# Kernel optimization log

Measured on AMD Instinct MI355X. Metric: run time of the kernel, lower is better.

The kernel has to match this reference:

```python
import jax, jax.numpy as jnp
import numpy as np

B, N, K, C, CM = 4, 1024, 9, 32, 128
SIGMA = 1.0
EPS = 1e-5
SLOPE = 0.01  # LeakyReLU default negative slope


def _batchnorm(x, gamma, beta):
    # training-mode BatchNorm1d over the point dimension
    m = x.mean(axis=0)
    v = x.var(axis=0)
    return gamma * (x - m) * jax.lax.rsqrt(v + EPS) + beta


def setup_inputs() -> dict:
    key = jax.random.key(0)
    ks = jax.random.split(key, 8)
    positions = jax.random.uniform(ks[0], (B * N, 2), jnp.float32) * 10.0
    weights = jax.random.normal(ks[1], (B * N, C), jnp.float32)
    # learned kernel offsets (grid-init in original; random offsets of same scale here)
    kernel_pos = jax.random.normal(ks[2], (K, 2), jnp.float32) * (2.0 * SIGMA)
    conv_w = jax.random.normal(ks[3], (K, C, C), jnp.float32) / np.sqrt(K * C)
    w1 = jax.random.normal(ks[4], (C, CM), jnp.float32) / np.sqrt(C)
    w2 = jax.random.normal(ks[5], (CM, C), jnp.float32) / np.sqrt(CM)
    return {
        "positions": positions,
        "weights": weights,
        "kernel_pos": kernel_pos,
        "conv_w": conv_w,
        "bn_gamma": jnp.ones((C,), jnp.float32),
        "bn_beta": jnp.zeros((C,), jnp.float32),
        "w1": w1,
        "b1": jnp.zeros((CM,), jnp.float32),
        "bn1_gamma": jnp.ones((CM,), jnp.float32),
        "bn1_beta": jnp.zeros((CM,), jnp.float32),
        "w2": w2,
        "b2": jnp.zeros((C,), jnp.float32),
        "n_batch": B,
        "n_points": N,
    }


def reference(positions, weights, kernel_pos, conv_w, bn_gamma, bn_beta,
              w1, b1, bn1_gamma, bn1_beta, w2, b2, n_batch, n_points):
    b, n = n_batch, n_points
    k = kernel_pos.shape[0]
    c = weights.shape[-1]
    pos = positions.reshape(b, n, 2)
    w = weights.reshape(b, n, c)

    # KernelConv: each component spawns K shifted components with channel mixing
    comp_pos = pos[:, :, None, :] + kernel_pos[None, None, :, :]      # [b,n,k,2]
    comp_w = jnp.einsum('bnc,kcd->bnkd', w, conv_w)                   # [b,n,k,c]

    # KernelSample: evaluate the resulting Gaussian mixture at the input positions
    diff = pos[:, :, None, None, :] - comp_pos[:, None, :, :, :]      # [b,i,n,k,2]
    dist2 = jnp.sum(diff * diff, axis=-1)                             # [b,i,n,k]
    kmat = jnp.exp(-dist2 / (2.0 * SIGMA * SIGMA))
    y = jnp.einsum('bink,bnkc->bic', kmat, comp_w)                    # [b,i,c]
    y = jax.nn.leaky_relu(y, SLOPE)
    y = y.reshape(b * n, c)

    # conv_norm + residual add of input weights
    y = _batchnorm(y, bn_gamma, bn_beta)
    y = y + weights

    # PyG MLP [C, CM, C], act_first=True, plain_last=True
    h = y @ w1 + b1
    h = jax.nn.leaky_relu(h, SLOPE)
    h = _batchnorm(h, bn1_gamma, bn1_beta)
    delta = h @ w2 + b2

    return y + delta  # output weights [b*n, c]; positions pass through unchanged
```

## Files before the change

kernel.cpp:

```cpp
#include <hip/hip_runtime.h>

#define BB 4
#define NN 1024
#define KK 9
#define C  32
#define CM 128
#define M  (BB*NN)
#define EPSB 1e-5f
#define SLOPE 0.01f

#define KPAD 296
#define WTS  40
#define GST  296
#define CWS  288

typedef _Float16 f16x8 __attribute__((ext_vector_type(8)));
typedef _Float16 f16x4 __attribute__((ext_vector_type(4)));
typedef float    f32x4 __attribute__((ext_vector_type(4)));

__device__ __forceinline__ float leaky(float x){ return x > 0.f ? x : SLOPE*x; }

__device__ __forceinline__ float fexp2(float x){
#if __has_builtin(__builtin_amdgcn_exp2f)
  return __builtin_amdgcn_exp2f(x);
#else
  return exp2f(x);
#endif
}

__global__ __launch_bounds__(512) void k2_main(const float* __restrict__ pos,
                                               const float* __restrict__ wts,
                                               const float* __restrict__ kpos,
                                               const float* __restrict__ conv_w,
                                               float* __restrict__ z,
                                               float* __restrict__ zpart,
                                               float* __restrict__ stats){
  __shared__ __align__(16) char smem[57984];
  _Float16* wT0 = (_Float16*)smem;
  float*    pnl = (float*)(smem + 5120);
  _Float16* km0 = (_Float16*)(smem + 13312);
  float* gld  = (float*)smem;
  float* cwT  = (float*)(smem + 18944);
  float* red2 = (float*)(smem + 55808);

  int bid = blockIdx.x;
  int b = bid >> 6, it = bid & 63;
  int tid = threadIdx.x;
  int lane = tid & 63, wid = tid >> 6;
  int mm = lane & 15, quad = lane >> 4;
  int c0 = (wid & 1) * 16, q = wid >> 1;
  int gk = tid >> 7, ig = (tid >> 3) & 15, np = tid & 7;
  int wn = tid >> 4, wc = (tid & 15) * 2;

  if (bid == 0){ for (int i = tid; i < 256; i += 512) stats[i] = 0.f; }

  const float BETA = -0.72134752f;
  float Ak[KK], Bk[KK], Ck[KK];
  #pragma unroll
  for (int k = 0; k < KK; ++k){
    float kxx = kpos[2*k], kyy = kpos[2*k+1];
    Ak[k] = -2.f*BETA*kxx;
    Bk[k] = -2.f*BETA*kyy;
    Ck[k] = BETA*(kxx*kxx + kyy*kyy);
  }

  const float2* wch = (const float2*)(wts + (size_t)b*NN*C);

#define WWRITE(dst, L) do{ \
    (dst)[wc*WTS + wn]     = (_Float16)(L).x; \
    (dst)[(wc+1)*WTS + wn] = (_Float16)(L).y; \
  }while(0)

#define GEN(dst, ss) do{ \
    float dx_[4], dy_[4], e0_[4]; \
    _Pragma("unroll") \
    for (int jj = 0; jj < 4; ++jj){ \
      int nl_ = np*4 + jj; \
      dx_[jj] = pix - pnl[2*((ss)*32 + nl_)]; \
      dy_[jj] = piy - pnl[2*((ss)*32 + nl_) + 1]; \
      e0_[jj] = BETA*(dx_[jj]*dx_[jj] + dy_[jj]*dy_[jj]); \
    } \
    _Pragma("unroll") \
    for (int t_ = 0; t_ < 3; ++t_){ \
      int k_ = gk + t_*4; \
      if (k_ < KK){ \
        f16x4 ev_; \
        _Pragma("unroll") \
        for (int jj = 0; jj < 4; ++jj){ \
          float x_ = (e0_[jj] + Ck[k_]) + dx_[jj]*Ak[k_] + dy_[jj]*Bk[k_]; \
          ev_[jj] = (_Float16)fexp2(x_); \
        } \
        *(f16x4*)&(dst)[ig*KPAD + k_*32 + np*4] = ev_; \
      } \
    } \
  }while(0)

  ((float4*)pnl)[tid] = ((const float4*)(pos + (size_t)b*NN*2))[tid];
  float2 L0 = wch[tid];
  float2 Ln = wch[512 + tid];
  WWRITE(wT0, L0);
  __syncthreads();
  float pix = pnl[2*(it*16 + ig)];
  float piy = pnl[2*(it*16 + ig) + 1];
  GEN(km0, 0);
  asm volatile("s_waitcnt lgkmcnt(0)" ::: "memory");
  __builtin_amdgcn_s_barrier();
  __builtin_amdgcn_sched_barrier(0);

  f32x4 acc0 = {0.f,0.f,0.f,0.f}, acc1 = {0.f,0.f,0.f,0.f}, acc2 = {0.f,0.f,0.f,0.f};
  for (int s = 0; s < 32; ++s){
    int cur = s & 1;
    if (s < 31){
      float2 Lw = Ln;
      if (s < 30) Ln = wch[(size_t)(s+2)*512 + tid];
      _Float16* wTn = wT0 + (cur^1)*(32*WTS);
      WWRITE(wTn, Lw);
      _Float16* kmn = km0 + (cur^1)*(16*KPAD);
      GEN(kmn, s+1);
    }
    const _Float16* kmc = km0 + cur*(16*KPAD);
    const _Float16* wTc = wT0 + cur*(32*WTS);
    f16x8 bf = *(const f16x8*)&wTc[(c0+mm)*WTS + quad*8];
    f16x8 a0 = *(const f16x8*)&kmc[mm*KPAD + (q+0)*32 + quad*8];
    acc0 = __builtin_amdgcn_mfma_f32_16x16x32_f16(a0, bf, acc0, 0, 0, 0);
    f16x8 a1 = *(const f16x8*)&kmc[mm*KPAD + (q+4)*32 + quad*8];
    acc1 = __builtin_amdgcn_mfma_f32_16x16x32_f16(a1, bf, acc1, 0, 0, 0);
    if (q == 0){
      f16x8 a2 = *(const f16x8*)&kmc[mm*KPAD + 8*32 + quad*8];
      acc2 = __builtin_amdgcn_mfma_f32_16x16x32_f16(a2, bf, acc2, 0, 0, 0);
    }
    asm volatile("s_waitcnt lgkmcnt(0)" ::: "memory");
    __builtin_amdgcn_sched_barrier(0);
    __builtin_amdgcn_s_barrier();
    __builtin_amdgcn_sched_barrier(0);
  }
#undef WWRITE
#undef GEN

  #pragma unroll
  for (int r = 0; r < 4; ++r){
    gld[(quad*4+r)*GST + (q+0)*32 + c0+mm] = acc0[r];
    gld[(quad*4+r)*GST + (q+4)*32 + c0+mm] = acc1[r];
  }
  if (q == 0){
    #pragma unroll
    for (int r = 0; r < 4; ++r)
      gld[(quad*4+r)*GST + 8*32 + c0+mm] = acc2[r];
  }
  for (int v = tid; v < (KK*C*C)/4; v += 512){
    float4 cv = ((const float4*)conv_w)[v];
    int f = v*4;
    int kc = f >> 5;
    int cb = f & 31;
    int q4 = kc >> 2, sub = kc & 3;
    #pragma unroll
    for (int j = 0; j < 4; ++j){
      int c = cb + j;
      cwT[c*CWS + ((q4 ^ (c & 7))<<2) + sub] = (&cv.x)[j];
    }
  }
  __syncthreads();

  int rr = tid >> 5, cc = tid & 31;
  const float4* g4 = (const float4*)&gld[rr*GST];
  const float4* w4 = (const float4*)&cwT[cc*CWS];
  int sw = cc & 7;
  f32x4 ya = {0.f,0.f,0.f,0.f}, yb = {0.f,0.f,0.f,0.f};
  for (int k = 0; k < KK; ++k){
    #pragma unroll
    for (int c4 = 0; c4 < 8; c4 += 2){
      float4 gv = g4[k*8 + c4];
      float4 wv = w4[(k*8 + c4) ^ sw];
      ya[0] += gv.x*wv.x; ya[1] += gv.y*wv.y; ya[2] += gv.z*wv.z; ya[3] += gv.w*wv.w;
      float4 gv2 = g4[k*8 + c4 + 1];
      float4 wv2 = w4[(k*8 + c4 + 1) ^ sw];
      yb[0] += gv2.x*wv2.x; yb[1] += gv2.y*wv2.y; yb[2] += gv2.z*wv2.z; yb[3] += gv2.w*wv2.w;
    }
  }
  float yv = (ya[0]+ya[1]) + (ya[2]+ya[3]) + (yb[0]+yb[1]) + (yb[2]+yb[3]);
  yv = leaky(yv);
  z[((size_t)b*NN + it*16 + rr)*C + cc] = yv;
  red2[cc*17 + rr] = yv;
  __syncthreads();
  if (tid < C){
    float s1 = 0.f, s2 = 0.f;
    #pragma unroll
    for (int r = 0; r < 16; ++r){ float t = red2[tid*17 + r]; s1 += t; s2 += t*t; }
    zpart[tid*256 + bid]            = s1;
    zpart[32*256 + tid*256 + bid]   = s2;
  }
}

__global__ __launch_bounds__(256) void k4_mlp1(const float* __restrict__ z,
                                               const float* __restrict__ weights,
                                               const float* __restrict__ bn_g,
                                               const float* __restrict__ bn_b,
                                               const float* __restrict__ w1,
                                               const float* __restrict__ b1,
                                               const float* __restrict__ zpart,
                                               float* __restrict__ stats,
                                               float* __restrict__ y,
                                               float* __restrict__ h){
  __shared__ float w1l[C*CM];
  __shared__ float yl[8*C];
  __shared__ float lt1[CM], lt2[CM];
  __shared__ float zs[2][8][32];
  __shared__ float zf[2][32];
  int tid = threadIdx.x;
  int row0 = blockIdx.x * 8;
  for (int v = tid; v < C*CM/4; v += 256)
    ((float4*)w1l)[v] = ((const float4*)w1)[v];
  if (tid < CM){ lt1[tid]=0.f; lt2[tid]=0.f; }
  {
    int c = tid & 31, seg = tid >> 5;
    const float4* p1 = (const float4*)&zpart[c*256 + seg*32];
    const float4* p2 = (const float4*)&zpart[8192 + c*256 + seg*32];
    float s1 = 0.f, s2 = 0.f;
    #pragma unroll
    for (int j = 0; j < 8; ++j){
      float4 a = p1[j]; s1 += (a.x+a.y)+(a.z+a.w);
      float4 d = p2[j]; s2 += (d.x+d.y)+(d.z+d.w);
    }
    zs[0][seg][c] = s1; zs[1][seg][c] = s2;
  }
  __syncthreads();
  if (tid < 64){
    int st = tid >> 5, c = tid & 31;
    float s = 0.f;
    #pragma unroll
    for (int g = 0; g < 8; ++g) s += zs[st][g][c];
    zf[st][c] = s;
  }
  __syncthreads();
  {
    int c  = tid & (C-1);
    int rl = tid >> 5;
    float mean = zf[0][c] * (1.f/M);
    float var  = zf[1][c] * (1.f/M) - mean*mean;
    float sc = bn_g[c] * rsqrtf(var + EPSB);
    float sh = bn_b[c] - mean*sc;
    int row = row0 + rl;
    float v = z[(size_t)row*C + c]*sc + sh + weights[(size_t)row*C + c];
    yl[tid] = v;
    y[(size_t)row*C + c] = v;
  }
  __syncthreads();
  {
    int col = tid & (CM-1);
    float la1 = 0.f, la2 = 0.f;
    #pragma unroll
    for (int j = 0; j < 4; ++j){
      int e = tid + j*256;
      int rl  = e >> 7;
      float acc = b1[col];
      #pragma unroll
      for (int c = 0; c < C; ++c) acc += yl[rl*C + c] * w1l[c*CM + col];
      acc = leaky(acc);
      h[(size_t)(row0+rl)*CM + col] = acc;
      la1 += acc; la2 += acc*acc;
    }
    atomicAdd(&lt1[col], la1);
    atomicAdd(&lt2[col], la2);
  }
  __syncthreads();
  if (tid < CM){
    atomicAdd(&stats[tid],      lt1[tid]);
    atomicAdd(&stats[CM + tid], lt2[tid]);
  }
}

__global__ __launch_bounds__(256) void k5_mlp2(const float* __restrict__ h,
                                               const float* __restrict__ y,
                                               const float* __restrict__ bn1_g,
                                               const float* __restrict__ bn1_b,
                                               const float* __restrict__ w2,
                                               const float* __restrict__ b2,
                                               const float* __restrict__ stats,
                                               float* __restrict__ out){
  __shared__ float w2l[CM*C];
  __shared__ float hl[8*CM];
  int tid = threadIdx.x;
  int row0 = blockIdx.x * 8;
  for (int v = tid; v < CM*C/4; v += 256)
    ((float4*)w2l)[v] = ((const float4*)w2)[v];
  {
    int col = tid & (CM-1);
    float t1 = stats[col], t2 = stats[CM + col];
    float mean = t1*(1.f/M);
    float var  = t2*(1.f/M) - mean*mean;
    float sc = bn1_g[col]*rsqrtf(var + EPSB);
    float sh = bn1_b[col] - mean*sc;
    #pragma unroll
    for (int j = 0; j < 4; ++j){
      int e = tid + j*256;
      int rl  = e >> 7;
      hl[e] = h[(size_t)(row0+rl)*CM + col]*sc + sh;
    }
  }
  __syncthreads();
  {
    int c  = tid & (C-1);
    int rl = tid >> 5;
    float acc = b2[c];
    #pragma unroll
    for (int jj = 0; jj < CM; ++jj) acc += hl[rl*CM + jj] * w2l[jj*C + c];
    int row = row0 + rl;
    out[(size_t)row*C + c] = y[(size_t)row*C + c] + acc;
  }
}

extern "C" void kernel_launch(void* const* d_in, const int* in_sizes, int n_in,
                              void* d_out, int out_size, void* d_ws, size_t ws_size,
                              hipStream_t stream) {
  const float* positions = (const float*)d_in[0];
  const float* weights   = (const float*)d_in[1];
  const float* kpos      = (const float*)d_in[2];
  const float* conv_w    = (const float*)d_in[3];
  const float* bn_g      = (const float*)d_in[4];
  const float* bn_b      = (const float*)d_in[5];
  const float* w1        = (const float*)d_in[6];
  const float* b1        = (const float*)d_in[7];
  const float* bn1_g     = (const float*)d_in[8];
  const float* bn1_b     = (const float*)d_in[9];
  const float* w2        = (const float*)d_in[10];
  const float* b2        = (const float*)d_in[11];
  float* out = (float*)d_out;

  float* ws = (float*)d_ws;
  float* z     = ws;
  float* y     = ws + 131072;
  float* h     = ws + 262144;
  float* zpart = ws + 786432;
  float* stats = ws + 802816;

  k2_main<<<256, 512, 0, stream>>>(positions, weights, kpos, conv_w, z, zpart, stats);
  k4_mlp1<<<M/8, 256, 0, stream>>>(z, weights, bn_g, bn_b, w1, b1, zpart, stats, y, h);
  k5_mlp2<<<M/8, 256, 0, stream>>>(h, y, bn1_g, bn1_b, w2, b2, stats, out);
}
```

Before: 129.5 us.

## Use split-fp16 MFMA for channel mixing and both MLP matmuls

Replaces the scalar FP32 dot-product loops in the conv channel-mixing stage, MLP layer 1 and MLP layer 2 with MFMA 16x16x32 f16 instructions. Each operand is split into hi and lo fp16 parts, and three products are summed to stay close to fp32 accuracy. The MLP kernels now handle 16 rows per block. The hidden activation is stored as hi/lo fp16 in MFMA fragment order, and the BN1 scale and shift are folded into w2 and the bias. This trades extra LDS traffic and conversion work for far fewer VALU FMAs, and the fp16 splitting (limited exponent range) adds some accuracy risk.

```diff
diff --git a/kernel.cpp b/kernel.cpp
--- a/kernel.cpp
+++ b/kernel.cpp
@@ -11,8 +11,8 @@
 
 #define KPAD 296
 #define WTS  40
-#define GST  296
-#define CWS  288
+#define GAP  296
+#define HPAD 136
 
 typedef _Float16 f16x8 __attribute__((ext_vector_type(8)));
 typedef _Float16 f16x4 __attribute__((ext_vector_type(4)));
@@ -35,13 +35,16 @@
                                                float* __restrict__ z,
                                                float* __restrict__ zpart,
                                                float* __restrict__ stats){
-  __shared__ __align__(16) char smem[57984];
+  __shared__ __align__(16) char smem[67200];
   _Float16* wT0 = (_Float16*)smem;
   float*    pnl = (float*)(smem + 5120);
   _Float16* km0 = (_Float16*)(smem + 13312);
-  float* gld  = (float*)smem;
-  float* cwT  = (float*)(smem + 18944);
-  float* red2 = (float*)(smem + 55808);
+  _Float16* gAh = (_Float16*)smem;
+  _Float16* gAl = (_Float16*)(smem + 9472);
+  _Float16* cwBh = (_Float16*)(smem + 18944);
+  _Float16* cwBl = (_Float16*)(smem + 37888);
+  float* red  = (float*)(smem + 56832);
+  float* red2 = (float*)(smem + 65024);
 
   int bid = blockIdx.x;
   int b = bid >> 6, it = bid & 63;
@@ -139,55 +142,73 @@
 
   #pragma unroll
   for (int r = 0; r < 4; ++r){
-    gld[(quad*4+r)*GST + (q+0)*32 + c0+mm] = acc0[r];
-    gld[(quad*4+r)*GST + (q+4)*32 + c0+mm] = acc1[r];
-  }
-  if (q == 0){
-    #pragma unroll
-    for (int r = 0; r < 4; ++r)
-      gld[(quad*4+r)*GST + 8*32 + c0+mm] = acc2[r];
+    int row = quad*4 + r;
+    float v0 = acc0[r];
+    _Float16 h0 = (_Float16)v0;
+    gAh[row*GAP + (q+0)*32 + c0+mm] = h0;
+    gAl[row*GAP + (q+0)*32 + c0+mm] = (_Float16)(v0 - (float)h0);
+    float v1 = acc1[r];
+    _Float16 h1 = (_Float16)v1;
+    gAh[row*GAP + (q+4)*32 + c0+mm] = h1;
+    gAl[row*GAP + (q+4)*32 + c0+mm] = (_Float16)(v1 - (float)h1);
+    if (q == 0){
+      float v2 = acc2[r];
+      _Float16 h2 = (_Float16)v2;
+      gAh[row*GAP + 8*32 + c0+mm] = h2;
+      gAl[row*GAP + 8*32 + c0+mm] = (_Float16)(v2 - (float)h2);
+    }
   }
   for (int v = tid; v < (KK*C*C)/4; v += 512){
     float4 cv = ((const float4*)conv_w)[v];
     int f = v*4;
-    int kc = f >> 5;
+    int k  = f >> 10;
+    int cp = (f >> 5) & 31;
     int cb = f & 31;
-    int q4 = kc >> 2, sub = kc & 3;
     #pragma unroll
     for (int j = 0; j < 4; ++j){
+      float x = (&cv.x)[j];
+      _Float16 hi = (_Float16)x;
       int c = cb + j;
-      cwT[c*CWS + ((q4 ^ (c & 7))<<2) + sub] = (&cv.x)[j];
-    }
-  }
-  __syncthreads();
-
-  int rr = tid >> 5, cc = tid & 31;
-  const float4* g4 = (const float4*)&gld[rr*GST];
-  const float4* w4 = (const float4*)&cwT[cc*CWS];
-  int sw = cc & 7;
-  f32x4 ya = {0.f,0.f,0.f,0.f}, yb = {0.f,0.f,0.f,0.f};
-  for (int k = 0; k < KK; ++k){
-    #pragma unroll
-    for (int c4 = 0; c4 < 8; c4 += 2){
-      float4 gv = g4[k*8 + c4];
-      float4 wv = w4[(k*8 + c4) ^ sw];
-      ya[0] += gv.x*wv.x; ya[1] += gv.y*wv.y; ya[2] += gv.z*wv.z; ya[3] += gv.w*wv.w;
-      float4 gv2 = g4[k*8 + c4 + 1];
-      float4 wv2 = w4[(k*8 + c4 + 1) ^ sw];
-      yb[0] += gv2.x*wv2.x; yb[1] += gv2.y*wv2.y; yb[2] += gv2.z*wv2.z; yb[3] += gv2.w*wv2.w;
-    }
-  }
-  float yv = (ya[0]+ya[1]) + (ya[2]+ya[3]) + (yb[0]+yb[1]) + (yb[2]+yb[3]);
-  yv = leaky(yv);
-  z[((size_t)b*NN + it*16 + rr)*C + cc] = yv;
-  red2[cc*17 + rr] = yv;
+      cwBh[c*GAP + k*32 + cp] = hi;
+      cwBl[c*GAP + k*32 + cp] = (_Float16)(x - (float)hi);
+    }
+  }
+  __syncthreads();
+
+  f32x4 yacc = {0.f,0.f,0.f,0.f};
+  #pragma unroll
+  for (int t = 0; t < 3; ++t){
+    int ks = q + t*4;
+    if (ks < KK){
+      f16x8 ah = *(const f16x8*)&gAh[mm*GAP + ks*32 + quad*8];
+      f16x8 al = *(const f16x8*)&gAl[mm*GAP + ks*32 + quad*8];
+      f16x8 bh = *(const f16x8*)&cwBh[(c0+mm)*GAP + ks*32 + quad*8];
+      f16x8 bl = *(const f16x8*)&cwBl[(c0+mm)*GAP + ks*32 + quad*8];
+      yacc = __builtin_amdgcn_mfma_f32_16x16x32_f16(ah, bh, yacc, 0, 0, 0);
+      yacc = __builtin_amdgcn_mfma_f32_16x16x32_f16(al, bh, yacc, 0, 0, 0);
+      yacc = __builtin_amdgcn_mfma_f32_16x16x32_f16(ah, bl, yacc, 0, 0, 0);
+    }
+  }
+  #pragma unroll
+  for (int r = 0; r < 4; ++r) red[wid*256 + (quad*4+r)*16 + mm] = yacc[r];
+  __syncthreads();
+  {
+    int rr = tid >> 5, cc = tid & 31;
+    int half = cc >> 4, c15 = cc & 15;
+    int o = rr*16 + c15;
+    float yv = red[(0+half)*256 + o] + red[(2+half)*256 + o]
+             + red[(4+half)*256 + o] + red[(6+half)*256 + o];
+    yv = leaky(yv);
+    z[((size_t)b*NN + it*16 + rr)*C + cc] = yv;
+    red2[cc*17 + rr] = yv;
+  }
   __syncthreads();
   if (tid < C){
     float s1 = 0.f, s2 = 0.f;
     #pragma unroll
     for (int r = 0; r < 16; ++r){ float t = red2[tid*17 + r]; s1 += t; s2 += t*t; }
-    zpart[tid*256 + bid]            = s1;
-    zpart[32*256 + tid*256 + bid]   = s2;
+    zpart[tid*256 + bid]          = s1;
+    zpart[32*256 + tid*256 + bid] = s2;
   }
 }
 
@@ -200,17 +221,16 @@
                                                const float* __restrict__ zpart,
                                                float* __restrict__ stats,
                                                float* __restrict__ y,
-                                               float* __restrict__ h){
-  __shared__ float w1l[C*CM];
-  __shared__ float yl[8*C];
-  __shared__ float lt1[CM], lt2[CM];
+                                               _Float16* __restrict__ hhl){
+  __shared__ __align__(16) _Float16 yAh[16*WTS], yAl[16*WTS];
+  __shared__ __align__(16) _Float16 w1Bh[CM*WTS], w1Bl[CM*WTS];
+  __shared__ float lt1[CM], lt2[CM], b1l[CM];
   __shared__ float zs[2][8][32];
   __shared__ float zf[2][32];
   int tid = threadIdx.x;
-  int row0 = blockIdx.x * 8;
-  for (int v = tid; v < C*CM/4; v += 256)
-    ((float4*)w1l)[v] = ((const float4*)w1)[v];
-  if (tid < CM){ lt1[tid]=0.f; lt2[tid]=0.f; }
+  int lane = tid & 63, wid = tid >> 6, mm = lane & 15, quad = lane >> 4;
+  int row0 = blockIdx.x * 16;
+
   {
     int c = tid & 31, seg = tid >> 5;
     const float4* p1 = (const float4*)&zpart[c*256 + seg*32];
@@ -223,6 +243,8 @@
     }
     zs[0][seg][c] = s1; zs[1][seg][c] = s2;
   }
+  if (tid < CM){ lt1[tid]=0.f; lt2[tid]=0.f; }
+  if (tid >= 128) b1l[tid-128] = b1[tid-128];
   __syncthreads();
   if (tid < 64){
     int st = tid >> 5, c = tid & 31;
@@ -232,35 +254,60 @@
     zf[st][c] = s;
   }
   __syncthreads();
-  {
-    int c  = tid & (C-1);
-    int rl = tid >> 5;
+
+  #pragma unroll
+  for (int e = tid; e < 512; e += 256){
+    int c = e & 31, rl = e >> 5;
     float mean = zf[0][c] * (1.f/M);
     float var  = zf[1][c] * (1.f/M) - mean*mean;
     float sc = bn_g[c] * rsqrtf(var + EPSB);
     float sh = bn_b[c] - mean*sc;
     int row = row0 + rl;
     float v = z[(size_t)row*C + c]*sc + sh + weights[(size_t)row*C + c];
-    yl[tid] = v;
     y[(size_t)row*C + c] = v;
-  }
-  __syncthreads();
-  {
-    int col = tid & (CM-1);
+    _Float16 hi = (_Float16)v;
+    yAh[rl*WTS + c] = hi;
+    yAl[rl*WTS + c] = (_Float16)(v - (float)hi);
+  }
+  for (int v = tid; v < (C*CM)/4; v += 256){
+    float4 t = ((const float4*)w1)[v];
+    int c = v >> 5, col = (v & 31)*4;
+    #pragma unroll
+    for (int j = 0; j < 4; ++j){
+      float x = (&t.x)[j];
+      _Float16 hi = (_Float16)x;
+      w1Bh[(col+j)*WTS + c] = hi;
+      w1Bl[(col+j)*WTS + c] = (_Float16)(x - (float)hi);
+    }
+  }
+  __syncthreads();
+
+  f16x8 ah = *(const f16x8*)&yAh[mm*WTS + quad*8];
+  f16x8 al = *(const f16x8*)&yAl[mm*WTS + quad*8];
+  #pragma unroll
+  for (int t2 = 0; t2 < 2; ++t2){
+    int ct = wid*2 + t2;
+    f16x8 bh = *(const f16x8*)&w1Bh[(ct*16+mm)*WTS + quad*8];
+    f16x8 bl = *(const f16x8*)&w1Bl[(ct*16+mm)*WTS + quad*8];
+    f32x4 acc = {0.f,0.f,0.f,0.f};
+    acc = __builtin_amdgcn_mfma_f32_16x16x32_f16(ah, bh, acc, 0, 0, 0);
+    acc = __builtin_amdgcn_mfma_f32_16x16x32_f16(al, bh, acc, 0, 0, 0);
+    acc = __builtin_amdgcn_mfma_f32_16x16x32_f16(ah, bl, acc, 0, 0, 0);
+    float bias = b1l[ct*16+mm];
     float la1 = 0.f, la2 = 0.f;
-    #pragma unroll
-    for (int j = 0; j < 4; ++j){
-      int e = tid + j*256;
-      int rl  = e >> 7;
-      float acc = b1[col];
-      #pragma unroll
-      for (int c = 0; c < C; ++c) acc += yl[rl*C + c] * w1l[c*CM + col];
-      acc = leaky(acc);
-      h[(size_t)(row0+rl)*CM + col] = acc;
-      la1 += acc; la2 += acc*acc;
-    }
-    atomicAdd(&lt1[col], la1);
-    atomicAdd(&lt2[col], la2);
+    f16x4 phi, plo;
+    #pragma unroll
+    for (int r = 0; r < 4; ++r){
+      float v = leaky(acc[r] + bias);
+      la1 += v; la2 += v*v;
+      _Float16 hi = (_Float16)v;
+      phi[r] = hi; plo[r] = (_Float16)(v - (float)hi);
+    }
+    atomicAdd(&lt1[ct*16+mm], la1);
+    atomicAdd(&lt2[ct*16+mm], la2);
+    size_t base = ((size_t)(blockIdx.x*256 + tid)*2 + t2)*4;
+    *(f16x4*)&hhl[base] = phi;
+    *(f16x4*)&hhl[(size_t)M*CM + base] = plo;
   }
   __syncthreads();
   if (tid < CM){
@@ -269,7 +316,7 @@
   }
 }
 
-__global__ __launch_bounds__(256) void k5_mlp2(const float* __restrict__ h,
+__global__ __launch_bounds__(256) void k5_mlp2(const _Float16* __restrict__ hhl,
                                                const float* __restrict__ y,
                                                const float* __restrict__ bn1_g,
                                                const float* __restrict__ bn1_b,
@@ -277,35 +324,85 @@
                                                const float* __restrict__ b2,
                                                const float* __restrict__ stats,
                                                float* __restrict__ out){
-  __shared__ float w2l[CM*C];
-  __shared__ float hl[8*CM];
+  __shared__ __align__(16) _Float16 hAh[16*HPAD], hAl[16*HPAD];
+  __shared__ __align__(16) _Float16 w2Bh[C*HPAD], w2Bl[C*HPAD];
+  __shared__ float ssc[CM], ssh[CM];
+  __shared__ float bl2[C];
+  __shared__ float red[4*256];
   int tid = threadIdx.x;
-  int row0 = blockIdx.x * 8;
-  for (int v = tid; v < CM*C/4; v += 256)
-    ((float4*)w2l)[v] = ((const float4*)w2)[v];
-  {
-    int col = tid & (CM-1);
-    float t1 = stats[col], t2 = stats[CM + col];
+  int lane = tid & 63, wid = tid >> 6, mm = lane & 15, quad = lane >> 4;
+  int row0 = blockIdx.x * 16;
+
+  size_t hb = ((size_t)(blockIdx.x*256 + tid)*2)*4;
+  f16x4 h0 = *(const f16x4*)&hhl[hb];
+  f16x4 h1 = *(const f16x4*)&hhl[hb + 4];
+  f16x4 l0 = *(const f16x4*)&hhl[(size_t)M*CM + hb];
+  f16x4 l1 = *(const f16x4*)&hhl[(size_t)M*CM + hb + 4];
+
+  if (tid < CM){
+    float t1 = stats[tid], t2 = stats[CM + tid];
     float mean = t1*(1.f/M);
     float var  = t2*(1.f/M) - mean*mean;
-    float sc = bn1_g[col]*rsqrtf(var + EPSB);
-    float sh = bn1_b[col] - mean*sc;
-    #pragma unroll
-    for (int j = 0; j < 4; ++j){
-      int e = tid + j*256;
-      int rl  = e >> 7;
-      hl[e] = h[(size_t)(row0+rl)*CM + col]*sc + sh;
-    }
-  }
-  __syncthreads();
-  {
-    int c  = tid & (C-1);
-    int rl = tid >> 5;
-    float acc = b2[c];
-    #pragma unroll
-    for (int jj = 0; jj < CM; ++jj) acc += hl[rl*CM + jj] * w2l[jj*C + c];
-    int row = row0 + rl;
-    out[(size_t)row*C + c] = y[(size_t)row*C + c] + acc;
+    float sc = bn1_g[tid]*rsqrtf(var + EPSB);
+    ssc[tid] = sc;
+    ssh[tid] = bn1_b[tid] - mean*sc;
+  }
+  if (tid >= 128 && tid < 160) bl2[tid-128] = b2[tid-128];
+
+  #pragma unroll
+  for (int t2 = 0; t2 < 2; ++t2){
+    int col = (wid*2 + t2)*16 + mm;
+    #pragma unroll
+    for (int r = 0; r < 4; ++r){
+      int row = quad*4 + r;
+      hAh[row*HPAD + col] = t2 ? h1[r] : h0[r];
+      hAl[row*HPAD + col] = t2 ? l1[r] : l0[r];
+    }
+  }
+  __syncthreads();
+
+  for (int v = tid; v < (CM*C)/4; v += 256){
+    float4 t = ((const float4*)w2)[v];
+    int j = v >> 3, c4 = (v & 7)*4;
+    float scj = ssc[j], shj = ssh[j];
+    #pragma unroll
+    for (int jj = 0; jj < 4; ++jj){
+      float x = (&t.x)[jj];
+      int c = c4 + jj;
+      atomicAdd(&bl2[c], shj * x);
+      float xp = x * scj;
+      _Float16 hi = (_Float16)xp;
+      w2Bh[c*HPAD + j] = hi;
+      w2Bl[c*HPAD + j] = (_Float16)(xp - (float)hi);
+    }
+  }
+  __syncthreads();
+
+  int ct = wid & 1, kh = wid >> 1;
+  f32x4 acc = {0.f,0.f,0.f,0.f};
+  #pragma unroll
+  for (int ks2 = 0; ks2 < 2; ++ks2){
+    int ks = kh*2 + ks2;
+    f16x8 ah = *(const f16x8*)&hAh[mm*HPAD + ks*32 + quad*8];
+    f16x8 al = *(const f16x8*)&hAl[mm*HPAD + ks*32 + quad*8];
+    f16x8 bh = *(const f16x8*)&w2Bh[(ct*16+mm)*HPAD + ks*32 + quad*8];
+    f16x8 bl = *(const f16x8*)&w2Bl[(ct*16+mm)*HPAD + ks*32 + quad*8];
+    acc = __builtin_amdgcn_mfma_f32_16x16x32_f16(ah, bh, acc, 0, 0, 0);
+    acc = __builtin_amdgcn_mfma_f32_16x16x32_f16(al, bh, acc, 0, 0, 0);
+    acc = __builtin_amdgcn_mfma_f32_16x16x32_f16(ah, bl, acc, 0, 0, 0);
+  }
+  #pragma unroll
+  for (int r = 0; r < 4; ++r) red[wid*256 + (quad*4+r)*16 + mm] = acc[r];
+  __syncthreads();
+
+  #pragma unroll
+  for (int e = tid; e < 512; e += 256){
+    int rr = e >> 5, cc = e & 31;
+    int half = cc >> 4;
+    int o = rr*16 + (cc & 15);
+    float val = red[half*256 + o] + red[(2+half)*256 + o];
+    int row = row0 + rr;
+    out[(size_t)row*C + cc] = y[(size_t)row*C + cc] + bl2[cc] + val;
   }
 }
 
@@ -327,13 +424,13 @@
   float* out = (float*)d_out;
 
   float* ws = (float*)d_ws;
-  float* z     = ws;
-  float* y     = ws + 131072;
-  float* h     = ws + 262144;
-  float* zpart = ws + 786432;
-  float* stats = ws + 802816;
+  float* z       = ws;
+  float* y       = ws + 131072;
+  _Float16* hhl  = (_Float16*)(ws + 262144);
+  float* zpart   = ws + 786432;
+  float* stats   = ws + 802816;
 
   k2_main<<<256, 512, 0, stream>>>(positions, weights, kpos, conv_w, z, zpart, stats);
-  k4_mlp1<<<M/8, 256, 0, stream>>>(z, weights, bn_g, bn_b, w1, b1, zpart, stats, y, h);
-  k5_mlp2<<<M/8, 256, 0, stream>>>(h, y, bn1_g, bn1_b, w2, b2, stats, out);
+  k4_mlp1<<<256, 256, 0, stream>>>(z, weights, bn_g, bn_b, w1, b1, zpart, stats, y, hhl);
+  k5_mlp2<<<256, 256, 0, stream>>>(hhl, y, bn1_g, bn1_b, w2, b2, stats, out);
 }
```

Result: faster. 124.2 us (-4.1%).
